# Optimization experiments

Measured on AMD Instinct MI355X. Metric: run time of the kernel, lower is better.

The kernel has to match this reference:

```python
import jax, jax.numpy as jnp
import numpy as np


def _binarize_kernel_wise(w):
    # Bi-ViT LinearBi (Qmodes.kernel_wise): per-output-channel scale alpha = mean(|w|)
    # quantized weight w_q = alpha * sign(w).  w: [out, in]
    alpha = jnp.mean(jnp.abs(w), axis=1, keepdims=True)  # [out, 1]
    return alpha * jnp.sign(w)


def setup_inputs() -> dict:
    key = jax.random.key(0)
    k_x, k_w1, k_b1, k_w2, k_b2 = jax.random.split(key, 5)
    B, N, C, H = 64, 197, 768, 3072
    x = jax.random.normal(k_x, (B, N, C), dtype=jnp.float32)
    w1 = jax.random.normal(k_w1, (H, C), dtype=jnp.float32) * 0.02
    b1 = jax.random.normal(k_b1, (H,), dtype=jnp.float32) * 0.02
    w2 = jax.random.normal(k_w2, (C, H), dtype=jnp.float32) * 0.02
    b2 = jax.random.normal(k_b2, (C,), dtype=jnp.float32) * 0.02
    return {"x": x, "w1": w1, "b1": b1, "w2": w2, "b2": b2}


def reference(x, w1, b1, w2, b2):
    # fc1 (binarized linear, kernel-wise scales)
    w1_q = _binarize_kernel_wise(w1)
    h = jnp.einsum('bnc,hc->bnh', x, w1_q) + b1
    # GELU (exact, erf-based as torch nn.GELU default) then clip to [-10, 10]
    h = jnp.clip(jax.nn.gelu(h, approximate=False), -10.0, 10.0)
    # dropout p=0.0 -> identity
    w2_q = _binarize_kernel_wise(w2)
    out = jnp.einsum('bnh,ch->bnc', h, w2_q) + b2
    return out
```

## Files before the change

### kernel.cpp

```cpp
#include <hip/hip_runtime.h>
#include <hip/hip_bf16.h>
#include <cstdint>
#include <cstddef>


typedef __bf16 bf16x8 __attribute__((ext_vector_type(8)));
typedef __bf16 bf16x4 __attribute__((ext_vector_type(4)));
typedef float floatx4 __attribute__((ext_vector_type(4)));

__device__ __forceinline__ void async_load16(const void* g, void* l) {
    __builtin_amdgcn_global_load_lds(
        (const __attribute__((address_space(1))) void*)g,
        (__attribute__((address_space(3))) void*)l,
        16, 0, 0);
}

__global__ __launch_bounds__(256) void prep_all(
    const float* __restrict__ x,
    const float* __restrict__ w1,
    const float* __restrict__ w2,
    __hip_bfloat16* __restrict__ xb,
    __hip_bfloat16* __restrict__ sgn1, float* __restrict__ alpha1,
    __hip_bfloat16* __restrict__ sgn2, float* __restrict__ alpha2,
    int nx8, int NBX)
{
    const int b = blockIdx.x;
    const int tid = threadIdx.x;
    if (b < NBX) {
        const float4* xv = (const float4*)x;
        bf16x8* xo = (bf16x8*)xb;
        const int stride = NBX * 256;
        for (int i = b * 256 + tid; i < nx8; i += stride) {
            float4 a = xv[2 * i];
            float4 c = xv[2 * i + 1];
            bf16x8 o;
            o[0] = (__bf16)a.x; o[1] = (__bf16)a.y;
            o[2] = (__bf16)a.z; o[3] = (__bf16)a.w;
            o[4] = (__bf16)c.x; o[5] = (__bf16)c.y;
            o[6] = (__bf16)c.z; o[7] = (__bf16)c.w;
            xo[i] = o;
        }
        return;
    }
    const int lane = tid & 63;
    const int wv = tid >> 6;
    const int wr = (b - NBX) * 4 + wv;
    const float* w; __hip_bfloat16* sgn; float* alpha; int cols4; int row;
    if (wr < 3072) {
        w = w1; sgn = sgn1; alpha = alpha1; cols4 = 192; row = wr;
    } else {
        w = w2; sgn = sgn2; alpha = alpha2; cols4 = 768; row = wr - 3072;
    }
    const float4* wrp = (const float4*)w + (size_t)row * cols4;
    bf16x4* sr = (bf16x4*)sgn + (size_t)row * cols4;
    float s = 0.0f;
    for (int c = lane; c < cols4; c += 64) {
        float4 v = wrp[c];
        s += fabsf(v.x) + fabsf(v.y) + fabsf(v.z) + fabsf(v.w);
        bf16x4 o;
        o[0] = (__bf16)(v.x > 0.0f ? 1.0f : (v.x < 0.0f ? -1.0f : 0.0f));
        o[1] = (__bf16)(v.y > 0.0f ? 1.0f : (v.y < 0.0f ? -1.0f : 0.0f));
        o[2] = (__bf16)(v.z > 0.0f ? 1.0f : (v.z < 0.0f ? -1.0f : 0.0f));
        o[3] = (__bf16)(v.w > 0.0f ? 1.0f : (v.w < 0.0f ? -1.0f : 0.0f));
        sr[c] = o;
    }
    #pragma unroll
    for (int off = 32; off > 0; off >>= 1) s += __shfl_down(s, off, 64);
    if (lane == 0) alpha[row] = s / (float)(cols4 * 4);
}

__device__ __forceinline__ void store_val(__hip_bfloat16* C, size_t idx, float v) {
    C[idx] = __float2bfloat16(v);
}
__device__ __forceinline__ void store_val(float* C, size_t idx, float v) {
    C[idx] = v;
}

template <bool DO_GELU, typename OutT>
__global__ __launch_bounds__(256) void gemm_bin(
    const __hip_bfloat16* __restrict__ A,
    const __hip_bfloat16* __restrict__ S,
    const float* __restrict__ alpha,
    const float* __restrict__ bias,
    OutT* __restrict__ C,
    int M, int N, int K, int T, int perXcd)
{
    constexpr int TM = 128;
    constexpr int TN = 128;
    constexpr int TK = 64;

    const int b = blockIdx.x;
    const int l = (b & 7) * perXcd + (b >> 3);
    if (l >= T) return;
    const int NT = N / TN;
    const int mt = l / NT;
    const int nt = l - mt * NT;
    const int bm = mt * TM;
    const int bn = nt * TN;

    __shared__ __align__(16) __hip_bfloat16 sA[TM * TK];
    __shared__ __align__(16) __hip_bfloat16 sB[TN * TK];

    const int tid = threadIdx.x;
    const int wave = tid >> 6;
    const int lane = tid & 63;

    const int wm = (wave & 1) * 64;
    const int wn = (wave >> 1) * 64;
    const int lr = lane & 15;
    const int kq = lane >> 4;
    const int e3 = lr & 7;

    const int crow = lane >> 3;
    const int ccol = ((lane & 7) ^ crow) * 8;

    floatx4 acc[4][4];
    #pragma unroll
    for (int i = 0; i < 4; i++)
        #pragma unroll
        for (int j = 0; j < 4; j++)
            #pragma unroll
            for (int r = 0; r < 4; r++)
                acc[i][j][r] = 0.0f;

    for (int k0 = 0; k0 < K; k0 += TK) {
        #pragma unroll
        for (int t = 0; t < 8; t++) {
            const int seg = wave * 8 + t;
            if (seg < 16) {
                const int r = seg * 8 + crow;
                int ar = bm + r;
                ar = ar < M ? ar : (M - 1);
                async_load16(A + (size_t)ar * K + (k0 + ccol), (void*)(sA + seg * 512));
            } else {
                const int r = (seg - 16) * 8 + crow;
                async_load16(S + (size_t)(bn + r) * K + (k0 + ccol),
                             (void*)(sB + (seg - 16) * 512));
            }
        }
        __syncthreads();

        #pragma unroll
        for (int ks = 0; ks < 2; ks++) {
            const int slot = ((ks << 2) | kq) ^ e3;
            bf16x8 af[4], bfv[4];
            #pragma unroll
            for (int i = 0; i < 4; i++)
                af[i] = *(const bf16x8*)(sA + (wm + i * 16 + lr) * TK + slot * 8);
            #pragma unroll
            for (int j = 0; j < 4; j++)
                bfv[j] = *(const bf16x8*)(sB + (wn + j * 16 + lr) * TK + slot * 8);
            #pragma unroll
            for (int i = 0; i < 4; i++)
                #pragma unroll
                for (int j = 0; j < 4; j++)
                    acc[i][j] = __builtin_amdgcn_mfma_f32_16x16x32_bf16(
                        af[i], bfv[j], acc[i][j], 0, 0, 0);
        }
        __syncthreads();
    }

    float al[4], bi[4];
    #pragma unroll
    for (int j = 0; j < 4; j++) {
        const int col = bn + wn + j * 16 + lr;
        al[j] = alpha[col];
        bi[j] = bias[col];
    }
    #pragma unroll
    for (int i = 0; i < 4; i++) {
        const int row0 = bm + wm + i * 16 + kq * 4;
        #pragma unroll
        for (int r = 0; r < 4; r++) {
            const int row = row0 + r;
            if (row < M) {
                #pragma unroll
                for (int j = 0; j < 4; j++) {
                    float v = acc[i][j][r] * al[j] + bi[j];
                    if (DO_GELU) {
                        v = 0.5f * v * (1.0f + erff(v * 0.70710678118654752f));
                        v = fminf(fmaxf(v, -10.0f), 10.0f);
                    }
                    store_val(C, (size_t)row * N + (bn + wn + j * 16 + lr), v);
                }
            }
        }
    }
}

extern "C" void kernel_launch(void* const* d_in, const int* in_sizes, int n_in,
                              void* d_out, int out_size, void* d_ws, size_t ws_size,
                              hipStream_t stream) {
    const float* x  = (const float*)d_in[0];
    const float* w1 = (const float*)d_in[1];
    const float* b1 = (const float*)d_in[2];
    const float* w2 = (const float*)d_in[3];
    const float* b2 = (const float*)d_in[4];

    const int M = 64 * 197;
    const int Cd = 768;
    const int Hd = 3072;

    char* ws = (char*)d_ws;
    __hip_bfloat16* xb   = (__hip_bfloat16*)ws;
    __hip_bfloat16* sgn1 = xb + (size_t)M * Cd;
    __hip_bfloat16* sgn2 = sgn1 + (size_t)Hd * Cd;
    float* alpha1 = (float*)(sgn2 + (size_t)Cd * Hd);
    float* alpha2 = alpha1 + Hd;
    __hip_bfloat16* hbuf = (__hip_bfloat16*)(alpha2 + Cd);

    const int nx8 = (M * Cd) / 8;
    const int NBX = 1280;
    const int NBW = (3072 + 768) / 4;
    prep_all<<<NBX + NBW, 256, 0, stream>>>(
        x, w1, w2, xb, sgn1, alpha1, sgn2, alpha2, nx8, NBX);

    const int gm = (M + 127) / 128;

    {
        const int T = (Hd / 128) * gm;
        const int perXcd = (T + 7) / 8;
        gemm_bin<true, __hip_bfloat16><<<perXcd * 8, 256, 0, stream>>>(
            xb, sgn1, alpha1, b1, hbuf, M, Hd, Cd, T, perXcd);
    }
    {
        const int T = (Cd / 128) * gm;
        const int perXcd = (T + 7) / 8;
        gemm_bin<false, float><<<perXcd * 8, 256, 0, stream>>>(
            hbuf, sgn2, alpha2, b2, (float*)d_out, M, Cd, Hd, T, perXcd);
    }
}
```

Measured before the change: 263.9 us.

## Double-buffer LDS tiles in binarized GEMM to overlap loads with MFMA

Moves GEMM tile staging into a dynamic shared buffer twice the size. The next K tile is issued asynchronously into the alternate buffer while MFMAs consume the current one. The aim is to hide global-to-LDS latency behind compute. In exchange, LDS per block doubles to 64KB, which may reduce resident blocks per CU.

```diff
diff --git a/kernel.cpp b/kernel.cpp
--- a/kernel.cpp
+++ b/kernel.cpp
@@ -89,6 +89,8 @@
     constexpr int TN = 128;
     constexpr int TK = 64;
 
+    extern __shared__ __align__(16) __hip_bfloat16 lds[];
+
     const int b = blockIdx.x;
     const int l = (b & 7) * perXcd + (b >> 3);
     if (l >= T) return;
@@ -98,9 +100,6 @@
     const int bm = mt * TM;
     const int bn = nt * TN;
 
-    __shared__ __align__(16) __hip_bfloat16 sA[TM * TK];
-    __shared__ __align__(16) __hip_bfloat16 sB[TN * TK];
-
     const int tid = threadIdx.x;
     const int wave = tid >> 6;
     const int lane = tid & 63;
@@ -114,16 +113,7 @@
     const int crow = lane >> 3;
     const int ccol = ((lane & 7) ^ crow) * 8;
 
-    floatx4 acc[4][4];
-    #pragma unroll
-    for (int i = 0; i < 4; i++)
-        #pragma unroll
-        for (int j = 0; j < 4; j++)
-            #pragma unroll
-            for (int r = 0; r < 4; r++)
-                acc[i][j][r] = 0.0f;
-
-    for (int k0 = 0; k0 < K; k0 += TK) {
+    auto STAGE = [&](int k0, __hip_bfloat16* dst) {
         #pragma unroll
         for (int t = 0; t < 8; t++) {
             const int seg = wave * 8 + t;
@@ -131,25 +121,48 @@
                 const int r = seg * 8 + crow;
                 int ar = bm + r;
                 ar = ar < M ? ar : (M - 1);
-                async_load16(A + (size_t)ar * K + (k0 + ccol), (void*)(sA + seg * 512));
+                async_load16(A + (size_t)ar * K + (k0 + ccol),
+                             (void*)(dst + seg * 512));
             } else {
                 const int r = (seg - 16) * 8 + crow;
                 async_load16(S + (size_t)(bn + r) * K + (k0 + ccol),
-                             (void*)(sB + (seg - 16) * 512));
+                             (void*)(dst + 8192 + (seg - 16) * 512));
             }
         }
-        __syncthreads();
-
+    };
+
+    floatx4 acc[4][4];
+    #pragma unroll
+    for (int i = 0; i < 4; i++)
+        #pragma unroll
+        for (int j = 0; j < 4; j++)
+            #pragma unroll
+            for (int r = 0; r < 4; r++)
+                acc[i][j][r] = 0.0f;
+
+    const int KT = K / TK;
+
+    STAGE(0, lds);
+    __syncthreads();
+
+    int p = 0;
+    for (int t = 0; t < KT; ++t) {
+        __hip_bfloat16* cur = lds + p * 16384;
+        if (t + 1 < KT)
+            STAGE((t + 1) * TK, lds + (p ^ 1) * 16384);
+
+        const __hip_bfloat16* cA = cur;
+        const __hip_bfloat16* cB = cur + 8192;
         #pragma unroll
         for (int ks = 0; ks < 2; ks++) {
             const int slot = ((ks << 2) | kq) ^ e3;
             bf16x8 af[4], bfv[4];
             #pragma unroll
             for (int i = 0; i < 4; i++)
-                af[i] = *(const bf16x8*)(sA + (wm + i * 16 + lr) * TK + slot * 8);
+                af[i] = *(const bf16x8*)(cA + (wm + i * 16 + lr) * TK + slot * 8);
             #pragma unroll
             for (int j = 0; j < 4; j++)
-                bfv[j] = *(const bf16x8*)(sB + (wn + j * 16 + lr) * TK + slot * 8);
+                bfv[j] = *(const bf16x8*)(cB + (wn + j * 16 + lr) * TK + slot * 8);
             #pragma unroll
             for (int i = 0; i < 4; i++)
                 #pragma unroll
@@ -157,7 +170,9 @@
                     acc[i][j] = __builtin_amdgcn_mfma_f32_16x16x32_bf16(
                         af[i], bfv[j], acc[i][j], 0, 0, 0);
         }
+
         __syncthreads();
+        p ^= 1;
     }
 
     float al[4], bi[4];
@@ -220,13 +235,19 @@
     {
         const int T = (Hd / 128) * gm;
         const int perXcd = (T + 7) / 8;
-        gemm_bin<true, __hip_bfloat16><<<perXcd * 8, 256, 0, stream>>>(
+        hipFuncSetAttribute(
+            reinterpret_cast<const void*>(&gemm_bin<true, __hip_bfloat16>),
+            hipFuncAttributeMaxDynamicSharedMemorySize, 65536);
+        gemm_bin<true, __hip_bfloat16><<<perXcd * 8, 256, 65536, stream>>>(
             xb, sgn1, alpha1, b1, hbuf, M, Hd, Cd, T, perXcd);
     }
     {
         const int T = (Cd / 128) * gm;
         const int perXcd = (T + 7) / 8;
-        gemm_bin<false, float><<<perXcd * 8, 256, 0, stream>>>(
+        hipFuncSetAttribute(
+            reinterpret_cast<const void*>(&gemm_bin<false, float>),
+            hipFuncAttributeMaxDynamicSharedMemorySize, 65536);
+        gemm_bin<false, float><<<perXcd * 8, 256, 65536, stream>>>(
             hbuf, sgn2, alpha2, b2, (float*)d_out, M, Cd, Hd, T, perXcd);
     }
 }
```

Result: slower. 272.1 us (+3.1%).
